# Kernel optimization log

Measured on AMD Instinct MI355X. Metric: run time of the kernel, lower is better.

Reference implementation:

```python
import jax, jax.numpy as jnp
import numpy as np

D = 448  # state_dim == input_dim == output_dim

def _param(key, shape):
    # matches torch.rand(shape) * 0.1 + 0.001
    return jax.random.uniform(key, shape, dtype=jnp.float32) * 0.1 + 0.001

def setup_inputs() -> dict:
    key = jax.random.key(0)
    ks = jax.random.split(key, 9)
    x = jax.random.normal(ks[0], (8, 4096, D), dtype=jnp.float32)
    return {
        "x": x,
        "W_q": _param(ks[1], (D, D)),
        "W_k": _param(ks[2], (D, D)),
        "W_v": _param(ks[3], (D, D)),
        "W_o": _param(ks[4], (D, D)),
        "SSM_A": _param(ks[5], (D, D)),
        "SSM_B": _param(ks[6], (D, D)),
        "SSM_C": _param(ks[7], (D, D)),
    }

def reference(x, W_q, W_k, W_v, W_o, SSM_A, SSM_B, SSM_C):
    # seq_len=4096 > threshold=256 -> quadratic SSM path.
    # structured_processing's einsum 'bsd,dd->bsd' multiplies elementwise by
    # the diagonal of the matrix; the block loop is redundant, so we apply the
    # diagonal scale over the whole sequence in one fused op.
    q = jnp.einsum('bsi,id->bsd', x, W_q)
    k = jnp.einsum('bsi,id->bsd', x, W_k)
    v = jnp.einsum('bsi,id->bsd', x, W_v)
    ssm = (q * jnp.diagonal(SSM_A)
           + k * jnp.diagonal(SSM_B)
           + v * jnp.diagonal(SSM_C))
    # dropout is identity in eval mode
    return jnp.einsum('bsd,do->bso', ssm, W_o)
```

## Files before the change

kernel.cpp:

```cpp
#include <hip/hip_runtime.h>
#include <hip/hip_bf16.h>

#define DDIM 448
#define NSTEP 14

typedef __hip_bfloat16 bf16;
typedef __attribute__((ext_vector_type(8))) short short8;
typedef __attribute__((ext_vector_type(4))) float f32x4;

__device__ __forceinline__ short bf_bits(float f) {
    bf16 h = __float2bfloat16(f);
    return *reinterpret_cast<short*>(&h);
}

__global__ __launch_bounds__(256) void prep_wc(
    const float* __restrict__ Wq, const float* __restrict__ Wk,
    const float* __restrict__ Wv, const float* __restrict__ Wo,
    const float* __restrict__ Ad, const float* __restrict__ Bd,
    const float* __restrict__ Cd, bf16* __restrict__ Wt)
{
    __shared__ __align__(16) bf16 As[64 * 32];
    __shared__ __align__(16) bf16 Bs[64 * 32];
    __shared__ float da[DDIM], db[DDIM], dc[DDIM];

    const int tid  = threadIdx.x;
    const int i0   = blockIdx.x * 64;
    const int o0   = blockIdx.y * 64;
    const int lane = tid & 63;
    const int wid  = tid >> 6;
    const int wm   = wid >> 1, wn = wid & 1;
    const int m_   = lane & 15, kq = lane >> 4;

    for (int d = tid; d < DDIM; d += 256) {
        da[d] = Ad[d * DDIM + d];
        db[d] = Bd[d * DDIM + d];
        dc[d] = Cd[d * DDIM + d];
    }

    const int dr  = tid >> 3;
    const int oc8 = (tid & 7) * 8;
    const int ir  = tid >> 2;
    const int dc8 = (tid & 3) * 8;

    f32x4 acc[2][2] = {};

    f32x4 w0 = *(const f32x4*)(Wo + dr * DDIM + o0 + oc8);
    f32x4 w1 = *(const f32x4*)(Wo + dr * DDIM + o0 + oc8 + 4);
    f32x4 q0 = *(const f32x4*)(Wq + (i0 + ir) * DDIM + dc8);
    f32x4 q1 = *(const f32x4*)(Wq + (i0 + ir) * DDIM + dc8 + 4);
    f32x4 t0 = *(const f32x4*)(Wk + (i0 + ir) * DDIM + dc8);
    f32x4 t1 = *(const f32x4*)(Wk + (i0 + ir) * DDIM + dc8 + 4);
    f32x4 v0 = *(const f32x4*)(Wv + (i0 + ir) * DDIM + dc8);
    f32x4 v1 = *(const f32x4*)(Wv + (i0 + ir) * DDIM + dc8 + 4);

    for (int k0 = 0; k0 < DDIM; k0 += 32) {
        __syncthreads();
        #pragma unroll
        for (int j = 0; j < 4; ++j) {
            As[(oc8 + j) * 32 + dr]     = __float2bfloat16(w0[j]);
            As[(oc8 + 4 + j) * 32 + dr] = __float2bfloat16(w1[j]);
        }
        short8 e;
        #pragma unroll
        for (int j = 0; j < 4; ++j) {
            e[j]     = bf_bits(q0[j] * da[k0 + dc8 + j]
                             + t0[j] * db[k0 + dc8 + j]
                             + v0[j] * dc[k0 + dc8 + j]);
            e[j + 4] = bf_bits(q1[j] * da[k0 + dc8 + 4 + j]
                             + t1[j] * db[k0 + dc8 + 4 + j]
                             + v1[j] * dc[k0 + dc8 + 4 + j]);
        }
        *(short8*)&Bs[ir * 32 + dc8] = e;
        __syncthreads();

        const int kn = (k0 + 32 < DDIM) ? k0 + 32 : 0;
        w0 = *(const f32x4*)(Wo + (kn + dr) * DDIM + o0 + oc8);
        w1 = *(const f32x4*)(Wo + (kn + dr) * DDIM + o0 + oc8 + 4);
        q0 = *(const f32x4*)(Wq + (i0 + ir) * DDIM + kn + dc8);
        q1 = *(const f32x4*)(Wq + (i0 + ir) * DDIM + kn + dc8 + 4);
        t0 = *(const f32x4*)(Wk + (i0 + ir) * DDIM + kn + dc8);
        t1 = *(const f32x4*)(Wk + (i0 + ir) * DDIM + kn + dc8 + 4);
        v0 = *(const f32x4*)(Wv + (i0 + ir) * DDIM + kn + dc8);
        v1 = *(const f32x4*)(Wv + (i0 + ir) * DDIM + kn + dc8 + 4);

        short8 af[2], bfr[2];
        #pragma unroll
        for (int mi = 0; mi < 2; ++mi)
            af[mi] = *(const short8*)&As[(wm * 32 + mi * 16 + m_) * 32 + kq * 8];
        #pragma unroll
        for (int ni = 0; ni < 2; ++ni)
            bfr[ni] = *(const short8*)&Bs[(wn * 32 + ni * 16 + m_) * 32 + kq * 8];
        #pragma unroll
        for (int mi = 0; mi < 2; ++mi)
            #pragma unroll
            for (int ni = 0; ni < 2; ++ni)
                acc[mi][ni] = __builtin_amdgcn_mfma_f32_16x16x32_bf16(
                    af[mi], bfr[ni], acc[mi][ni], 0, 0, 0);
    }

    #pragma unroll
    for (int mi = 0; mi < 2; ++mi)
        #pragma unroll
        for (int ni = 0; ni < 2; ++ni) {
            const int o = o0 + wm * 32 + mi * 16 + kq * 4;
            const int i = i0 + wn * 32 + ni * 16 + m_;
            bf16* dst = Wt + (i >> 5) * (DDIM * 32) + (i & 31);
            #pragma unroll
            for (int r = 0; r < 4; ++r)
                dst[(o + r) * 32] = __float2bfloat16(acc[mi][ni][r]);
        }
}

__global__ __launch_bounds__(512, 2) void gemm_xwc(
    const float* __restrict__ X, const bf16* __restrict__ Wt,
    float* __restrict__ out)
{
    __shared__ __align__(16) char smem[74240];

    const int tid  = threadIdx.x;
    const int lane = tid & 63;
    const int wid  = tid >> 6;
    const int wr   = wid >> 2;
    const int wc   = wid & 3;
    const int m_   = lane & 15;
    const int kq   = lane >> 4;
    const int row0 = blockIdx.x * 128;

    const int ar = tid >> 2;
    const int ac = (tid & 3) * 8;
    const float* agp = X + (row0 + ar) * DDIM + ac;

    const bf16* bgp = Wt + (wc * 112 + m_) * 32 + kq * 8;

    f32x4 acc[4][7] = {};
    short8 bA[7], bB[7];

    f32x4 a0 = *(const f32x4*)(agp);
    f32x4 a1 = *(const f32x4*)(agp + 4);
    {
        bf16* A0 = (bf16*)smem;
        short8 w;
        #pragma unroll
        for (int j = 0; j < 4; ++j) {
            w[j] = bf_bits(a0[j]); w[j + 4] = bf_bits(a1[j]);
        }
        *(short8*)&A0[ar * 32 + ac] = w;
    }
    a0 = *(const f32x4*)(agp + 32);
    a1 = *(const f32x4*)(agp + 36);
    #pragma unroll
    for (int j = 0; j < 7; ++j)
        bA[j] = *(const short8*)(bgp + j * 512);
    asm volatile("s_waitcnt lgkmcnt(0)" ::: "memory");
    __builtin_amdgcn_s_barrier();

#define GSTEP(S, BCUR, BNXT)                                                 \
    {                                                                        \
        const bf16* Ac = (const bf16*)(smem + (((S) & 1) << 13));            \
        if ((S) + 1 < NSTEP) {                                               \
            const bf16* bs = bgp + ((S) + 1) * (DDIM * 32);                  \
            _Pragma("unroll")                                                \
            for (int j = 0; j < 7; ++j)                                      \
                BNXT[j] = *(const short8*)(bs + j * 512);                    \
            bf16* An = (bf16*)(smem + ((((S) + 1) & 1) << 13));              \
            short8 w;                                                        \
            _Pragma("unroll")                                                \
            for (int j = 0; j < 4; ++j) {                                    \
                w[j] = bf_bits(a0[j]); w[j + 4] = bf_bits(a1[j]);            \
            }                                                                \
            *(short8*)&An[ar * 32 + ac] = w;                                 \
        }                                                                    \
        if ((S) + 2 < NSTEP) {                                               \
            a0 = *(const f32x4*)(agp + ((S) + 2) * 32);                      \
            a1 = *(const f32x4*)(agp + ((S) + 2) * 32 + 4);                  \
        }                                                                    \
        short8 af[4];                                                        \
        _Pragma("unroll")                                                    \
        for (int mi = 0; mi < 4; ++mi)                                       \
            af[mi] = *(const short8*)&Ac[(wr * 64 + mi * 16 + m_) * 32       \
                                         + kq * 8];                          \
        _Pragma("unroll")                                                    \
        for (int mi = 0; mi < 4; ++mi)                                       \
            _Pragma("unroll")                                                \
            for (int ni = 0; ni < 7; ++ni)                                   \
                acc[mi][ni] = __builtin_amdgcn_mfma_f32_16x16x32_bf16(       \
                    af[mi], BCUR[ni], acc[mi][ni], 0, 0, 0);                 \
        asm volatile("s_waitcnt lgkmcnt(0)" ::: "memory");                   \
        __builtin_amdgcn_s_barrier();                                        \
    }

    #pragma unroll
    for (int ss = 0; ss < NSTEP; ss += 2) {
        GSTEP(ss,     bA, bB)
        GSTEP(ss + 1, bB, bA)
    }
#undef GSTEP

    float* Cb = (float*)(smem + 16384);
    #pragma unroll
    for (int t = 0; t < 4; ++t) {
        if (wr == (t >> 1)) {
            #pragma unroll
            for (int mi2 = 0; mi2 < 2; ++mi2) {
                const int mi = (t & 1) * 2 + mi2;
                #pragma unroll
                for (int ni = 0; ni < 7; ++ni) {
                    const int col = wc * 112 + ni * 16 + m_;
                    #pragma unroll
                    for (int r = 0; r < 4; ++r)
                        Cb[(mi2 * 16 + kq * 4 + r) * 452 + col] = acc[mi][ni][r];
                }
            }
        }
        asm volatile("s_waitcnt lgkmcnt(0)" ::: "memory");
        __builtin_amdgcn_s_barrier();
        const f32x4* Cb4 = (const f32x4*)Cb;
        f32x4* dst4 = (f32x4*)(out + (row0 + t * 32) * DDIM);
        #pragma unroll
        for (int j = 0; j < 7; ++j) {
            const int v   = j * 512 + tid;
            const int row = v / 112;
            const int cw  = v - row * 112;
            dst4[v] = Cb4[row * 113 + cw];
        }
        asm volatile("s_waitcnt lgkmcnt(0)" ::: "memory");
        __builtin_amdgcn_s_barrier();
    }
}

extern "C" void kernel_launch(void* const* d_in, const int* in_sizes, int n_in,
                              void* d_out, int out_size, void* d_ws, size_t ws_size,
                              hipStream_t stream) {
    const float* x  = (const float*)d_in[0];
    const float* Wq = (const float*)d_in[1];
    const float* Wk = (const float*)d_in[2];
    const float* Wv = (const float*)d_in[3];
    const float* Wo = (const float*)d_in[4];
    const float* Ad = (const float*)d_in[5];
    const float* Bd = (const float*)d_in[6];
    const float* Cd = (const float*)d_in[7];

    bf16*  Wt  = (bf16*)d_ws;
    float* out = (float*)d_out;

    const int M = in_sizes[0] / DDIM;

    prep_wc<<<dim3(7, 7), 256, 0, stream>>>(Wq, Wk, Wv, Wo, Ad, Bd, Cd, Wt);
    gemm_xwc<<<M / 128, 512, 0, stream>>>(x, Wt, out);
}
```

Measured before the change: 145.2 us.

## Load X fragments directly into registers and drop shared-memory staging in GEMM

```diff
diff --git a/kernel.cpp b/kernel.cpp
--- a/kernel.cpp
+++ b/kernel.cpp
@@ -115,8 +115,6 @@
     const float* __restrict__ X, const bf16* __restrict__ Wt,
     float* __restrict__ out)
 {
-    __shared__ __align__(16) char smem[74240];
-
     const int tid  = threadIdx.x;
     const int lane = tid & 63;
     const int wid  = tid >> 6;
@@ -124,69 +122,61 @@
     const int wc   = wid & 3;
     const int m_   = lane & 15;
     const int kq   = lane >> 4;
-    const int row0 = blockIdx.x * 128;
-
-    const int ar = tid >> 2;
-    const int ac = (tid & 3) * 8;
-    const float* agp = X + (row0 + ar) * DDIM + ac;
-
-    const bf16* bgp = Wt + (wc * 112 + m_) * 32 + kq * 8;
+    const int row0 = blockIdx.x * 128 + wr * 64;
+
+    const float* axp = X + (row0 + m_) * DDIM + kq * 8;
+    const bf16* bxp = Wt + (wc * 112 + m_) * 32 + kq * 8;
 
     f32x4 acc[4][7] = {};
+    short8 af[4];
     short8 bA[7], bB[7];
-
-    f32x4 a0 = *(const f32x4*)(agp);
-    f32x4 a1 = *(const f32x4*)(agp + 4);
-    {
-        bf16* A0 = (bf16*)smem;
-        short8 w;
+    f32x4 a0[4], a1[4];
+
+    #pragma unroll
+    for (int mi = 0; mi < 4; ++mi) {
+        a0[mi] = *(const f32x4*)(axp + mi * 16 * DDIM);
+        a1[mi] = *(const f32x4*)(axp + mi * 16 * DDIM + 4);
+    }
+    #pragma unroll
+    for (int ni = 0; ni < 7; ++ni)
+        bA[ni] = *(const short8*)(bxp + ni * 512);
+    #pragma unroll
+    for (int mi = 0; mi < 4; ++mi)
         #pragma unroll
         for (int j = 0; j < 4; ++j) {
-            w[j] = bf_bits(a0[j]); w[j + 4] = bf_bits(a1[j]);
-        }
-        *(short8*)&A0[ar * 32 + ac] = w;
-    }
-    a0 = *(const f32x4*)(agp + 32);
-    a1 = *(const f32x4*)(agp + 36);
-    #pragma unroll
-    for (int j = 0; j < 7; ++j)
-        bA[j] = *(const short8*)(bgp + j * 512);
-    asm volatile("s_waitcnt lgkmcnt(0)" ::: "memory");
-    __builtin_amdgcn_s_barrier();
-
-#define GSTEP(S, BCUR, BNXT)                                                 \
-    {                                                                        \
-        const bf16* Ac = (const bf16*)(smem + (((S) & 1) << 13));            \
-        if ((S) + 1 < NSTEP) {                                               \
-            const bf16* bs = bgp + ((S) + 1) * (DDIM * 32);                  \
-            _Pragma("unroll")                                                \
-            for (int j = 0; j < 7; ++j)                                      \
-                BNXT[j] = *(const short8*)(bs + j * 512);                    \
-            bf16* An = (bf16*)(smem + ((((S) + 1) & 1) << 13));              \
-            short8 w;                                                        \
-            _Pragma("unroll")                                                \
-            for (int j = 0; j < 4; ++j) {                                    \
-                w[j] = bf_bits(a0[j]); w[j + 4] = bf_bits(a1[j]);            \
-            }                                                                \
-            *(short8*)&An[ar * 32 + ac] = w;                                 \
-        }                                                                    \
-        if ((S) + 2 < NSTEP) {                                               \
-            a0 = *(const f32x4*)(agp + ((S) + 2) * 32);                      \
-            a1 = *(const f32x4*)(agp + ((S) + 2) * 32 + 4);                  \
-        }                                                                    \
-        short8 af[4];                                                        \
-        _Pragma("unroll")                                                    \
-        for (int mi = 0; mi < 4; ++mi)                                       \
-            af[mi] = *(const short8*)&Ac[(wr * 64 + mi * 16 + m_) * 32       \
-                                         + kq * 8];                          \
-        _Pragma("unroll")                                                    \
-        for (int mi = 0; mi < 4; ++mi)                                       \
-            _Pragma("unroll")                                                \
-            for (int ni = 0; ni < 7; ++ni)                                   \
-                acc[mi][ni] = __builtin_amdgcn_mfma_f32_16x16x32_bf16(       \
-                    af[mi], BCUR[ni], acc[mi][ni], 0, 0, 0);                 \
-        asm volatile("s_waitcnt lgkmcnt(0)" ::: "memory");                   \
-        __builtin_amdgcn_s_barrier();                                        \
+            af[mi][j]     = bf_bits(a0[mi][j]);
+            af[mi][j + 4] = bf_bits(a1[mi][j]);
+        }
+
+#define GSTEP(S, BCUR, BNXT)                                                \
+    {                                                                       \
+        if ((S) + 1 < NSTEP) {                                              \
+            const bf16* bs = bxp + ((S) + 1) * (DDIM * 32);                 \
+            _Pragma("unroll")                                               \
+            for (int ni = 0; ni < 7; ++ni)                                  \
+                BNXT[ni] = *(const short8*)(bs + ni * 512);                 \
+            const float* as = axp + ((S) + 1) * 32;                         \
+            _Pragma("unroll")                                               \
+            for (int mi = 0; mi < 4; ++mi) {                                \
+                a0[mi] = *(const f32x4*)(as + mi * 16 * DDIM);              \
+                a1[mi] = *(const f32x4*)(as + mi * 16 * DDIM + 4);          \
+            }                                                               \
+        }                                                                   \
+        _Pragma("unroll")                                                   \
+        for (int mi = 0; mi < 4; ++mi)                                      \
+            _Pragma("unroll")                                               \
+            for (int ni = 0; ni < 7; ++ni)                                  \
+                acc[mi][ni] = __builtin_amdgcn_mfma_f32_16x16x32_bf16(      \
+                    af[mi], BCUR[ni], acc[mi][ni], 0, 0, 0);                \
+        if ((S) + 1 < NSTEP) {                                              \
+            _Pragma("unroll")                                               \
+            for (int mi = 0; mi < 4; ++mi)                                  \
+                _Pragma("unroll")                                           \
+                for (int j = 0; j < 4; ++j) {                               \
+                    af[mi][j]     = bf_bits(a0[mi][j]);                     \
+                    af[mi][j + 4] = bf_bits(a1[mi][j]);                     \
+                }                                                           \
+        }                                                                   \
     }
 
     #pragma unroll
@@ -196,35 +186,18 @@
     }
 #undef GSTEP
 
-    float* Cb = (float*)(smem + 16384);
-    #pragma unroll
-    for (int t = 0; t < 4; ++t) {
-        if (wr == (t >> 1)) {
+    {
+        const int crow = row0 + kq * 4;
+        const int ccol = wc * 112 + m_;
+        #pragma unroll
+        for (int mi = 0; mi < 4; ++mi)
             #pragma unroll
-            for (int mi2 = 0; mi2 < 2; ++mi2) {
-                const int mi = (t & 1) * 2 + mi2;
+            for (int ni = 0; ni < 7; ++ni) {
+                float* dst = out + (crow + mi * 16) * DDIM + ccol + ni * 16;
                 #pragma unroll
-                for (int ni = 0; ni < 7; ++ni) {
-                    const int col = wc * 112 + ni * 16 + m_;
-                    #pragma unroll
-                    for (int r = 0; r < 4; ++r)
-                        Cb[(mi2 * 16 + kq * 4 + r) * 452 + col] = acc[mi][ni][r];
-                }
+                for (int r = 0; r < 4; ++r)
+                    dst[r * DDIM] = acc[mi][ni][r];
             }
-        }
-        asm volatile("s_waitcnt lgkmcnt(0)" ::: "memory");
-        __builtin_amdgcn_s_barrier();
-        const f32x4* Cb4 = (const f32x4*)Cb;
-        f32x4* dst4 = (f32x4*)(out + (row0 + t * 32) * DDIM);
-        #pragma unroll
-        for (int j = 0; j < 7; ++j) {
-            const int v   = j * 512 + tid;
-            const int row = v / 112;
-            const int cw  = v - row * 112;
-            dst4[v] = Cb4[row * 113 + cw];
-        }
-        asm volatile("s_waitcnt lgkmcnt(0)" ::: "memory");
-        __builtin_amdgcn_s_barrier();
     }
 }
 
```

Measured after the change: 168.6 us. 1.16x slower.
